# Optimization experiments

Measured on AMD Instinct MI355X. Metric: run time of the kernel, lower is better.

## Reference

```python
import jax, jax.numpy as jnp
import numpy as np

B, D, L = 16, 64, 1280
H = 8            # nhead
WIN = 5          # window_size (divides L exactly)
DFF = 128        # dim_feedforward
EPS = 1e-5


def _layernorm(x, g, b):
    mu = jnp.mean(x, axis=-1, keepdims=True)
    var = jnp.mean(jnp.square(x - mu), axis=-1, keepdims=True)
    return (x - mu) * jax.lax.rsqrt(var + EPS) * g + b


def _mha(x, w_in, b_in, w_out, b_out):
    # x: (Bx, Lx, D). torch nn.MultiheadAttention, batch_first, eval mode.
    Bx, Lx, Dm = x.shape
    hd = Dm // H
    qkv = x @ w_in.T + b_in                      # (Bx, Lx, 3D)
    q, k, v = jnp.split(qkv, 3, axis=-1)
    q = q.reshape(Bx, Lx, H, hd)
    k = k.reshape(Bx, Lx, H, hd)
    v = v.reshape(Bx, Lx, H, hd)
    scale = 1.0 / jnp.sqrt(jnp.asarray(hd, x.dtype))
    scores = jnp.einsum('bqhd,bkhd->bhqk', q, k) * scale
    att = jax.nn.softmax(scores, axis=-1)
    out = jnp.einsum('bhqk,bkhd->bqhd', att, v).reshape(Bx, Lx, Dm)
    return out @ w_out.T + b_out


def setup_inputs() -> dict:
    key = jax.random.key(0)
    ks = jax.random.split(key, 16)
    s = 0.05
    return {
        'x': jax.random.normal(ks[0], (B, D, L), dtype=jnp.float32),
        # local attention params
        'lw_in': jax.random.normal(ks[1], (3 * D, D), dtype=jnp.float32) * s,
        'lb_in': jnp.zeros((3 * D,), jnp.float32),
        'lw_out': jax.random.normal(ks[2], (D, D), dtype=jnp.float32) * s,
        'lb_out': jnp.zeros((D,), jnp.float32),
        # global attention params
        'gw_in': jax.random.normal(ks[3], (3 * D, D), dtype=jnp.float32) * s,
        'gb_in': jnp.zeros((3 * D,), jnp.float32),
        'gw_out': jax.random.normal(ks[4], (D, D), dtype=jnp.float32) * s,
        'gb_out': jnp.zeros((D,), jnp.float32),
        # gating weight (init 0.5 like the module)
        'local_weight': jnp.full((D,), 0.5, jnp.float32),
        # layer norms
        'g1': jnp.ones((D,), jnp.float32), 'b1': jnp.zeros((D,), jnp.float32),
        'g2': jnp.ones((D,), jnp.float32), 'b2': jnp.zeros((D,), jnp.float32),
        'g3': jnp.ones((D,), jnp.float32), 'b3': jnp.zeros((D,), jnp.float32),
        # FFN
        'w1': jax.random.normal(ks[5], (DFF, D), dtype=jnp.float32) * s,
        'bf1': jnp.zeros((DFF,), jnp.float32),
        'w2': jax.random.normal(ks[6], (D, DFF), dtype=jnp.float32) * s,
        'bf2': jnp.zeros((D,), jnp.float32),
    }


def reference(x, lw_in, lb_in, lw_out, lb_out, gw_in, gb_in, gw_out, gb_out,
              local_weight, g1, b1, g2, b2, g3, b3, w1, bf1, w2, bf2):
    xt = jnp.transpose(x, (0, 2, 1))              # (B, L, D)
    residual = xt
    nW = L // WIN
    xw = xt.reshape(B * nW, WIN, D)
    local_out = _mha(xw, lw_in, lb_in, lw_out, lb_out).reshape(B, L, D)
    local_out = _layernorm(local_out + residual, g1, b1)
    # global attention
    global_out = _mha(xt, gw_in, gb_in, gw_out, gb_out)
    global_out = _layernorm(global_out + residual, g2, b2)
    # gated channel fusion
    alpha = jax.nn.sigmoid(local_weight)[None, None, :]
    fused = alpha * local_out + (1.0 - alpha) * global_out
    # FFN (dropout is identity in eval mode)
    ffn_out = jax.nn.relu(fused @ w1.T + bf1) @ w2.T + bf2
    out = _layernorm(ffn_out + fused, g3, b3)
    return jnp.transpose(out, (0, 2, 1))          # (B, D, L)
```

## Files before the change

kernel.cpp:

```cpp
#include <hip/hip_runtime.h>
#include <math.h>

typedef short bf16x8 __attribute__((ext_vector_type(8)));
typedef float f32x4 __attribute__((ext_vector_type(4)));
typedef float f32x16 __attribute__((ext_vector_type(16)));
typedef unsigned short u16;
typedef unsigned int u32;

#define RFL(x) __builtin_amdgcn_readfirstlane(x)

static __device__ __forceinline__ float bf2f(u16 s) {
  union { u32 u; float f; } c; c.u = ((u32)s) << 16; return c.f;
}
static __device__ __forceinline__ u16 f2bf(float f) {
  union { float f; u32 u; } c; c.f = f;
  u32 u = c.u + 0x7fffu + ((c.u >> 16) & 1u);
  return (u16)(u >> 16);
}
static __device__ __forceinline__ u32 pk2(float lo, float hi) {
  u32 r;
  asm("v_cvt_pk_bf16_f32 %0, %1, %2" : "=v"(r) : "v"(lo), "v"(hi));
  return r;
}
static __device__ __forceinline__ f32x4 MF(bf16x8 a, bf16x8 b, f32x4 c) {
  return __builtin_amdgcn_mfma_f32_16x16x32_bf16(a, b, c, 0, 0, 0);
}
static __device__ __forceinline__ f32x16 MF32(bf16x8 a, bf16x8 b, f32x16 c) {
  return __builtin_amdgcn_mfma_f32_32x32x16_bf16(a, b, c, 0, 0, 0);
}


__global__ __launch_bounds__(256) void qkvx(
    const float* __restrict__ x, const float* __restrict__ lw_in,
    const float* __restrict__ gw_in, const float* __restrict__ lb_in,
    const float* __restrict__ gb_in, u16* __restrict__ QKV) {
  __shared__ __align__(16) float xs[32][68];
  __shared__ __align__(16) u16 XTs[32 * 64];
  const int t = threadIdx.x;
  const int b = blockIdx.x / 40, l0 = (blockIdx.x % 40) * 32;
  for (int i = t; i < 2048; i += 256) {
    const int d = i >> 5, tok = i & 31;
    xs[tok][d] = x[(b * 64 + d) * 1280 + l0 + tok];
  }
  __syncthreads();
  {
    const int tok = t >> 3, c8 = (t & 7) * 8;
    union { bf16x8 v; u32 u[4]; } o;
    const float* src = &xs[tok][c8];
    o.u[0] = pk2(src[0], src[1]); o.u[1] = pk2(src[2], src[3]);
    o.u[2] = pk2(src[4], src[5]); o.u[3] = pk2(src[6], src[7]);
    const int byteoff = (tok * 128 + c8 * 2) ^ ((tok & 7) << 4);
    *(bf16x8*)((char*)XTs + byteoff) = o.v;
  }
  __syncthreads();
  const int lane = t & 63, w = RFL(t >> 6);
  const int lr = lane & 15, lg = lane >> 4;
  const int n0 = w * 96;
  bf16x8 a[2][2];
#pragma unroll
  for (int mt = 0; mt < 2; ++mt)
#pragma unroll
    for (int ks = 0; ks < 2; ++ks) {
      const int row = mt * 16 + lr;
      const int abyte = (row * 128 + ks * 64 + lg * 16) ^ ((row & 7) << 4);
      a[mt][ks] = *(const bf16x8*)((char*)XTs + abyte);
    }
  const float* W32 = (n0 < 192) ? lw_in : gw_in;
  const int nb = (n0 < 192) ? n0 : n0 - 192;
  bf16x8 bb[6][2];
#pragma unroll
  for (int nt = 0; nt < 6; ++nt)
#pragma unroll
    for (int ks = 0; ks < 2; ++ks) {
      const float* src = W32 + (nb + nt * 16 + lr) * 64 + ks * 32 + lg * 8;
      const float4 f0 = *(const float4*)src;
      const float4 f1 = *(const float4*)(src + 4);
      union { bf16x8 v; u32 u[4]; } o;
      o.u[0] = pk2(f0.x, f0.y); o.u[1] = pk2(f0.z, f0.w);
      o.u[2] = pk2(f1.x, f1.y); o.u[3] = pk2(f1.z, f1.w);
      bb[nt][ks] = o.v;
    }
  f32x4 acc[2][6];
#pragma unroll
  for (int mt = 0; mt < 2; ++mt)
#pragma unroll
    for (int nt = 0; nt < 6; ++nt) {
      f32x4 z = {0.f, 0.f, 0.f, 0.f};
      acc[mt][nt] = z;
#pragma unroll
      for (int ks = 0; ks < 2; ++ks)
        acc[mt][nt] = MF(a[mt][ks], bb[nt][ks], acc[mt][nt]);
    }
#pragma unroll
  for (int nt = 0; nt < 6; ++nt) {
    const int col = n0 + nt * 16 + lr;
    const float bias = (col < 192) ? lb_in[col] : gb_in[col - 192];
    const float scale = (col < 64) ? 0.35355339059327373f
                      : ((col >= 192 && col < 256) ? 0.51010407600615432f : 1.f);
#pragma unroll
    for (int mt = 0; mt < 2; ++mt)
#pragma unroll
      for (int r = 0; r < 4; ++r) {
        const int row = b * 1280 + l0 + mt * 16 + 4 * lg + r;
        QKV[row * 384 + col] = f2bf((acc[mt][nt][r] + bias) * scale);
      }
  }
}

__global__ __launch_bounds__(512) void attn(
    const u16* __restrict__ QKV, u16* __restrict__ AOl, u16* __restrict__ AOg,
    const float* __restrict__ lw_out, const float* __restrict__ gw_out,
    const float* __restrict__ w1, const float* __restrict__ w2,
    u16* __restrict__ Wlout, u16* __restrict__ Wgout,
    u16* __restrict__ W1b, u16* __restrict__ W2b) {
  __shared__ __align__(16) u16 Klds[1280 * 8];
  __shared__ __align__(16) u16 VT[9 * 1320];
  const int t = threadIdx.x;
  if (blockIdx.x < 5) {
    const int b = blockIdx.y >> 3, h = blockIdx.y & 7;
    for (int l = t; l < 1280; l += 512) {
      const int src = (b * 1280 + l) * 384 + h * 8;
      bf16x8 kv = *(const bf16x8*)(QKV + src + 256);
      bf16x8 vv = *(const bf16x8*)(QKV + src + 320);
      const int k5 = l & 31;
      const int pos = (l & ~31) +
                      ((k5 & 0x13) | ((k5 & 4) << 1) | ((k5 & 8) >> 1));
      *(bf16x8*)(Klds + pos * 8) = kv;
#pragma unroll
      for (int d = 0; d < 8; ++d) VT[d * 1320 + l] = (u16)vv[d];
    }
    for (int l = t; l < 1280; l += 512) VT[8 * 1320 + l] = 0x3F80;
    __syncthreads();
    const int lane = t & 63, w = RFL(t >> 6);
    const int c = lane & 31, hi = lane >> 5;
    const int q0 = blockIdx.x * 256 + w * 32;
    const int qrow = b * 1280 + q0 + c;
    const bf16x8 qv = *(const bf16x8*)(QKV + qrow * 384 + 192 + h * 8);
    const bf16x8 qz = {0, 0, 0, 0, 0, 0, 0, 0};
    const bf16x8 qf = (hi == 0) ? qv : qz;
    const u16* kp = Klds + c * 8;
    const int vrow = (c < 8) ? c : 8;
    const u16* vp = VT + vrow * 1320 + hi * 8;
    f32x16 oacc;
#pragma unroll
    for (int i = 0; i < 16; ++i) oacc[i] = 0.f;
    f32x16 z16;
#pragma unroll
    for (int i = 0; i < 16; ++i) z16[i] = 0.f;
#pragma unroll 2
    for (int jt = 0; jt < 40; ++jt) {
      bf16x8 kf = *(const bf16x8*)kp;
      f32x16 s = MF32(kf, qf, z16);
      float p[16];
#pragma unroll
      for (int i = 0; i < 16; ++i) p[i] = __builtin_amdgcn_exp2f(s[i]);
      union { u32 u[4]; bf16x8 v; } pb1, pb2;
      pb1.u[0] = pk2(p[0], p[1]);  pb1.u[1] = pk2(p[2], p[3]);
      pb1.u[2] = pk2(p[4], p[5]);  pb1.u[3] = pk2(p[6], p[7]);
      pb2.u[0] = pk2(p[8], p[9]);  pb2.u[1] = pk2(p[10], p[11]);
      pb2.u[2] = pk2(p[12], p[13]); pb2.u[3] = pk2(p[14], p[15]);
      bf16x8 vf1 = *(const bf16x8*)vp;
      oacc = MF32(vf1, pb1.v, oacc);
      bf16x8 vf2 = *(const bf16x8*)(vp + 16);
      oacc = MF32(vf2, pb2.v, oacc);
      kp += 256; vp += 32;
    }
    const float ssum = __shfl(oacc[4], c);
    const float inv = 1.f / ssum;
    const int base = qrow * 64 + h * 8 + hi * 4;
    *(u32*)(AOg + base) = pk2(oacc[0] * inv, oacc[1] * inv);
    *(u32*)(AOg + base + 2) = pk2(oacc[2] * inv, oacc[3] * inv);
    return;
  }
  const int lid = (blockIdx.x - 5) * 128 + blockIdx.y;
  if (lid < 320) {
    const int g = lid * 512 + t;
    const int qi = g % 5, h = (g / 5) & 7, wi = (g / 40) & 255, b = g / 10240;
    const int row = b * 1280 + wi * 5 + qi;
    float q[8];
    {
      bf16x8 qv = *(const bf16x8*)(QKV + row * 384 + h * 8);
#pragma unroll
      for (int d = 0; d < 8; ++d) q[d] = bf2f((u16)qv[d]);
    }
    float p[5], sum = 0.f;
#pragma unroll
    for (int j = 0; j < 5; ++j) {
      const int krow = b * 1280 + wi * 5 + j;
      bf16x8 kv = *(const bf16x8*)(QKV + krow * 384 + 64 + h * 8);
      float s = 0.f;
#pragma unroll
      for (int d = 0; d < 8; ++d) s = fmaf(q[d], bf2f((u16)kv[d]), s);
      p[j] = __expf(s); sum += p[j];
    }
    const float inv = 1.f / sum;
    float o[8] = {0, 0, 0, 0, 0, 0, 0, 0};
#pragma unroll
    for (int j = 0; j < 5; ++j) {
      const int vrow = b * 1280 + wi * 5 + j;
      bf16x8 vv = *(const bf16x8*)(QKV + vrow * 384 + 128 + h * 8);
#pragma unroll
      for (int d = 0; d < 8; ++d) o[d] = fmaf(p[j], bf2f((u16)vv[d]), o[d]);
    }
    union { bf16x8 v; u32 u[4]; } ov;
    ov.u[0] = pk2(o[0] * inv, o[1] * inv); ov.u[1] = pk2(o[2] * inv, o[3] * inv);
    ov.u[2] = pk2(o[4] * inv, o[5] * inv); ov.u[3] = pk2(o[6] * inv, o[7] * inv);
    *(bf16x8*)(AOl + row * 64 + h * 8) = ov.v;
  } else {
    const int f = (lid - 320) * 512 + t;
    if (f < 4096)       Wlout[f] = f2bf(lw_out[f]);
    else if (f < 8192)  Wgout[f - 4096] = f2bf(gw_out[f - 4096]);
    else if (f < 16384) W1b[f - 8192] = f2bf(w1[f - 8192]);
    else if (f < 24576) W2b[f - 16384] = f2bf(w2[f - 16384]);
  }
}

__global__ __launch_bounds__(64) void tail_kernel(
    const u16* __restrict__ AOl, const u16* __restrict__ AOg,
    const u16* __restrict__ Wlout, const u16* __restrict__ Wgout,
    const u16* __restrict__ W1b, const u16* __restrict__ W2b,
    const float* __restrict__ lb_out, const float* __restrict__ gb_out,
    const float* __restrict__ lwt,
    const float* __restrict__ g1, const float* __restrict__ b1,
    const float* __restrict__ g2, const float* __restrict__ b2,
    const float* __restrict__ g3, const float* __restrict__ b3,
    const float* __restrict__ bf1, const float* __restrict__ bf2,
    const float* __restrict__ x, float* __restrict__ out) {
  __shared__ __align__(16) float xso[64][20];
  __shared__ __align__(16) u16 Ft[16 * 64];
  __shared__ __align__(16) u16 Ht[16 * 128];
  const int t = threadIdx.x;
  const int b = blockIdx.y, l0 = blockIdx.x * 16;
  for (int i = t; i < 1024; i += 64) {
    const int d = i >> 4, tok = i & 15;
    xso[d][tok] = x[(b * 64 + d) * 1280 + l0 + tok];
  }
  __syncthreads();
  const int lr = t & 15, lg = (t & 63) >> 4;
  const int grow = b * 1280 + l0;

  f32x4 accl[4], accg[4];
#pragma unroll
  for (int nt = 0; nt < 4; ++nt) { f32x4 z = {0,0,0,0}; accl[nt] = z; accg[nt] = z; }
#pragma unroll
  for (int ks = 0; ks < 2; ++ks) {
    bf16x8 al = *(const bf16x8*)(AOl + (grow + lr) * 64 + ks * 32 + lg * 8);
    bf16x8 ag = *(const bf16x8*)(AOg + (grow + lr) * 64 + ks * 32 + lg * 8);
#pragma unroll
    for (int nt = 0; nt < 4; ++nt) {
      bf16x8 bl = *(const bf16x8*)(Wlout + (nt * 16 + lr) * 64 + ks * 32 + lg * 8);
      bf16x8 bg = *(const bf16x8*)(Wgout + (nt * 16 + lr) * 64 + ks * 32 + lg * 8);
      accl[nt] = MF(al, bl, accl[nt]);
      accg[nt] = MF(ag, bg, accg[nt]);
    }
  }
#pragma unroll
  for (int nt = 0; nt < 4; ++nt) {
    const int col = nt * 16 + lr;
    const float bl = lb_out[col], bg = gb_out[col];
    f32x4 xr = *(const f32x4*)&xso[col][lg * 4];
#pragma unroll
    for (int r = 0; r < 4; ++r) {
      accl[nt][r] += bl + xr[r];
      accg[nt][r] += bg + xr[r];
    }
  }
  auto LN = [&](f32x4* a, const float* gam, const float* bet) {
    float gv[4], bv[4];
#pragma unroll
    for (int nt = 0; nt < 4; ++nt) { gv[nt] = gam[nt * 16 + lr]; bv[nt] = bet[nt * 16 + lr]; }
#pragma unroll
    for (int r = 0; r < 4; ++r) {
      float s = a[0][r] + a[1][r] + a[2][r] + a[3][r];
      s += __shfl_xor(s, 1); s += __shfl_xor(s, 2);
      s += __shfl_xor(s, 4); s += __shfl_xor(s, 8);
      const float mu = s * 0.015625f;
      float q = 0.f;
#pragma unroll
      for (int nt = 0; nt < 4; ++nt) { const float cv = a[nt][r] - mu; q = fmaf(cv, cv, q); }
      q += __shfl_xor(q, 1); q += __shfl_xor(q, 2);
      q += __shfl_xor(q, 4); q += __shfl_xor(q, 8);
      const float rsq = rsqrtf(q * 0.015625f + 1e-5f);
#pragma unroll
      for (int nt = 0; nt < 4; ++nt)
        a[nt][r] = (a[nt][r] - mu) * rsq * gv[nt] + bv[nt];
    }
  };
  LN(accl, g1, b1);
  LN(accg, g2, b2);
  f32x4 fus[4];
#pragma unroll
  for (int nt = 0; nt < 4; ++nt) {
    const int col = nt * 16 + lr;
    const float al_ = 1.f / (1.f + __expf(-lwt[col]));
#pragma unroll
    for (int r = 0; r < 4; ++r)
      fus[nt][r] = al_ * accl[nt][r] + (1.f - al_) * accg[nt][r];
  }
#pragma unroll
  for (int nt = 0; nt < 4; ++nt)
#pragma unroll
    for (int r = 0; r < 4; ++r) {
      const int ltok = lg * 4 + r;
      const int byteoff = (ltok * 128 + (nt * 16 + lr) * 2) ^ ((ltok & 7) << 4);
      *(u16*)((char*)Ft + byteoff) = f2bf(fus[nt][r]);
    }
  asm volatile("" ::: "memory");
  __syncthreads();
  f32x4 hcc[8];
#pragma unroll
  for (int nt = 0; nt < 8; ++nt) { f32x4 z = {0,0,0,0}; hcc[nt] = z; }
#pragma unroll
  for (int ks = 0; ks < 2; ++ks) {
    const int abyte = (lr * 128 + ks * 64 + lg * 16) ^ ((lr & 7) << 4);
    bf16x8 af = *(const bf16x8*)((char*)Ft + abyte);
#pragma unroll
    for (int nt = 0; nt < 8; ++nt) {
      bf16x8 bw = *(const bf16x8*)(W1b + (nt * 16 + lr) * 64 + ks * 32 + lg * 8);
      hcc[nt] = MF(af, bw, hcc[nt]);
    }
  }
#pragma unroll
  for (int nt = 0; nt < 8; ++nt) {
    const int f = nt * 16 + lr;
    const float bbv = bf1[f];
#pragma unroll
    for (int r = 0; r < 4; ++r) {
      const float v = fmaxf(hcc[nt][r] + bbv, 0.f);
      const int ltok = lg * 4 + r;
      const int byteoff = (ltok * 256 + f * 2) ^ ((ltok & 7) << 4);
      *(u16*)((char*)Ht + byteoff) = f2bf(v);
    }
  }
  asm volatile("" ::: "memory");
  f32x4 occ[4];
#pragma unroll
  for (int nt = 0; nt < 4; ++nt) { f32x4 z = {0,0,0,0}; occ[nt] = z; }
#pragma unroll
  for (int ks = 0; ks < 4; ++ks) {
    const int abyte = (lr * 256 + ks * 64 + lg * 16) ^ ((lr & 7) << 4);
    bf16x8 af = *(const bf16x8*)((char*)Ht + abyte);
#pragma unroll
    for (int nt = 0; nt < 4; ++nt) {
      bf16x8 bw = *(const bf16x8*)(W2b + (nt * 16 + lr) * 128 + ks * 32 + lg * 8);
      occ[nt] = MF(af, bw, occ[nt]);
    }
  }
#pragma unroll
  for (int nt = 0; nt < 4; ++nt) {
    const float bb2 = bf2[nt * 16 + lr];
#pragma unroll
    for (int r = 0; r < 4; ++r) occ[nt][r] += bb2 + fus[nt][r];
  }
  LN(occ, g3, b3);
#pragma unroll
  for (int nt = 0; nt < 4; ++nt)
#pragma unroll
    for (int r = 0; r < 4; ++r)
      xso[nt * 16 + lr][lg * 4 + r] = occ[nt][r];
  __syncthreads();
  for (int i = t; i < 1024; i += 64) {
    const int d = i >> 4, tok = i & 15;
    out[(b * 64 + d) * 1280 + l0 + tok] = xso[d][tok];
  }
}

extern "C" void kernel_launch(void* const* d_in, const int* in_sizes, int n_in,
                              void* d_out, int out_size, void* d_ws,
                              size_t ws_size, hipStream_t stream) {
  const float* x      = (const float*)d_in[0];
  const float* lw_in  = (const float*)d_in[1];
  const float* lb_in  = (const float*)d_in[2];
  const float* lw_out = (const float*)d_in[3];
  const float* lb_out = (const float*)d_in[4];
  const float* gw_in  = (const float*)d_in[5];
  const float* gb_in  = (const float*)d_in[6];
  const float* gw_out = (const float*)d_in[7];
  const float* gb_out = (const float*)d_in[8];
  const float* lwt    = (const float*)d_in[9];
  const float* g1 = (const float*)d_in[10]; const float* b1 = (const float*)d_in[11];
  const float* g2 = (const float*)d_in[12]; const float* b2 = (const float*)d_in[13];
  const float* g3 = (const float*)d_in[14]; const float* b3 = (const float*)d_in[15];
  const float* w1 = (const float*)d_in[16]; const float* bf1 = (const float*)d_in[17];
  const float* w2 = (const float*)d_in[18]; const float* bf2 = (const float*)d_in[19];
  float* out = (float*)d_out;

  u16* QKV   = (u16*)d_ws;
  u16* AOl   = QKV + 7864320;
  u16* AOg   = AOl + 1310720;
  u16* Wlout = AOg + 1310720;
  u16* Wgout = Wlout + 4096;
  u16* W1b   = Wgout + 4096;
  u16* W2b   = W1b + 8192;

  qkvx<<<dim3(640), dim3(256), 0, stream>>>(x, lw_in, gw_in, lb_in, gb_in, QKV);
  attn<<<dim3(8, 128), dim3(512), 0, stream>>>(QKV, AOl, AOg, lw_out, gw_out,
                                               w1, w2, Wlout, Wgout, W1b, W2b);
  tail_kernel<<<dim3(80, 16), dim3(64), 0, stream>>>(
      AOl, AOg, Wlout, Wgout, W1b, W2b, lb_out, gb_out, lwt,
      g1, b1, g2, b2, g3, b3, bf1, bf2, x, out);
}
```

Before: 77.03 us.

## Split global attention over two key halves and merge partial sums in tail

The global attention is split into two key-range halves per (batch, head, query-block), with 256-thread blocks instead of 512. This gives more blocks and smaller LDS use per block. Each half writes unnormalized fp32 partial outputs and row sums to workspace. The tail kernel adds the two halves and normalizes them, which costs extra global traffic for the fp32 partials. The inner loop also alternates between two accumulators to break the MFMA dependency chain, and it skips the max-subtraction across splits just as before.

```diff
diff --git a/kernel.cpp b/kernel.cpp
--- a/kernel.cpp
+++ b/kernel.cpp
@@ -107,19 +107,23 @@
   }
 }
 
-__global__ __launch_bounds__(512) void attn(
-    const u16* __restrict__ QKV, u16* __restrict__ AOl, u16* __restrict__ AOg,
+__global__ __launch_bounds__(256) void attn(
+    const u16* __restrict__ QKV, u16* __restrict__ AOl,
+    float* __restrict__ OSUM, float* __restrict__ OACC8,
     const float* __restrict__ lw_out, const float* __restrict__ gw_out,
     const float* __restrict__ w1, const float* __restrict__ w2,
     u16* __restrict__ Wlout, u16* __restrict__ Wgout,
     u16* __restrict__ W1b, u16* __restrict__ W2b) {
-  __shared__ __align__(16) u16 Klds[1280 * 8];
-  __shared__ __align__(16) u16 VT[9 * 1320];
+  __shared__ __align__(16) u16 Klds[640 * 8];
+  __shared__ __align__(16) u16 VT[9 * 664];
   const int t = threadIdx.x;
-  if (blockIdx.x < 5) {
-    const int b = blockIdx.y >> 3, h = blockIdx.y & 7;
-    for (int l = t; l < 1280; l += 512) {
-      const int src = (b * 1280 + l) * 384 + h * 8;
+  if (blockIdx.x < 20) {
+    const int bh = blockIdx.y;
+    const int b = bh >> 3, h = bh & 7;
+    const int split = blockIdx.x & 1, qblk = blockIdx.x >> 1;
+    const int k0 = split * 640;
+    for (int l = t; l < 640; l += 256) {
+      const int src = (b * 1280 + k0 + l) * 384 + h * 8;
       bf16x8 kv = *(const bf16x8*)(QKV + src + 256);
       bf16x8 vv = *(const bf16x8*)(QKV + src + 320);
       const int k5 = l & 31;
@@ -127,28 +131,23 @@
                       ((k5 & 0x13) | ((k5 & 4) << 1) | ((k5 & 8) >> 1));
       *(bf16x8*)(Klds + pos * 8) = kv;
 #pragma unroll
-      for (int d = 0; d < 8; ++d) VT[d * 1320 + l] = (u16)vv[d];
-    }
-    for (int l = t; l < 1280; l += 512) VT[8 * 1320 + l] = 0x3F80;
+      for (int d = 0; d < 8; ++d) VT[d * 664 + l] = (u16)vv[d];
+    }
+    for (int l = t; l < 664; l += 256) VT[8 * 664 + l] = 0x3F80;
     __syncthreads();
     const int lane = t & 63, w = RFL(t >> 6);
     const int c = lane & 31, hi = lane >> 5;
-    const int q0 = blockIdx.x * 256 + w * 32;
-    const int qrow = b * 1280 + q0 + c;
-    const bf16x8 qv = *(const bf16x8*)(QKV + qrow * 384 + 192 + h * 8);
+    const int q = qblk * 128 + w * 32 + c;
+    const bf16x8 qv = *(const bf16x8*)(QKV + (b * 1280 + q) * 384 + 192 + h * 8);
     const bf16x8 qz = {0, 0, 0, 0, 0, 0, 0, 0};
     const bf16x8 qf = (hi == 0) ? qv : qz;
     const u16* kp = Klds + c * 8;
     const int vrow = (c < 8) ? c : 8;
-    const u16* vp = VT + vrow * 1320 + hi * 8;
-    f32x16 oacc;
-#pragma unroll
-    for (int i = 0; i < 16; ++i) oacc[i] = 0.f;
-    f32x16 z16;
-#pragma unroll
-    for (int i = 0; i < 16; ++i) z16[i] = 0.f;
-#pragma unroll 2
-    for (int jt = 0; jt < 40; ++jt) {
+    const u16* vp = VT + vrow * 664 + hi * 8;
+    f32x16 oaccA, oaccB, z16;
+#pragma unroll
+    for (int i = 0; i < 16; ++i) { oaccA[i] = 0.f; oaccB[i] = 0.f; z16[i] = 0.f; }
+    auto step = [&](f32x16& oacc) {
       bf16x8 kf = *(const bf16x8*)kp;
       f32x16 s = MF32(kf, qf, z16);
       float p[16];
@@ -164,17 +163,24 @@
       bf16x8 vf2 = *(const bf16x8*)(vp + 16);
       oacc = MF32(vf2, pb2.v, oacc);
       kp += 256; vp += 32;
-    }
-    const float ssum = __shfl(oacc[4], c);
-    const float inv = 1.f / ssum;
-    const int base = qrow * 64 + h * 8 + hi * 4;
-    *(u32*)(AOg + base) = pk2(oacc[0] * inv, oacc[1] * inv);
-    *(u32*)(AOg + base + 2) = pk2(oacc[2] * inv, oacc[3] * inv);
+    };
+#pragma unroll 2
+    for (int jt2 = 0; jt2 < 10; ++jt2) {
+      step(oaccA);
+      step(oaccB);
+    }
+    f32x16 oacc;
+#pragma unroll
+    for (int i = 0; i < 16; ++i) oacc[i] = oaccA[i] + oaccB[i];
+    const int qi = bh * 1280 + q;
+    if (hi == 0) OSUM[split * 163840 + qi] = oacc[4];
+    f32x4 od = {oacc[0], oacc[1], oacc[2], oacc[3]};
+    *(f32x4*)(OACC8 + split * 1310720 + qi * 8 + hi * 4) = od;
     return;
   }
-  const int lid = (blockIdx.x - 5) * 128 + blockIdx.y;
-  if (lid < 320) {
-    const int g = lid * 512 + t;
+  const int lid = (blockIdx.x - 20) * 128 + blockIdx.y;
+  if (lid < 640) {
+    const int g = lid * 256 + t;
     const int qi = g % 5, h = (g / 5) & 7, wi = (g / 40) & 255, b = g / 10240;
     const int row = b * 1280 + wi * 5 + qi;
     float q[8];
@@ -206,8 +212,8 @@
     ov.u[0] = pk2(o[0] * inv, o[1] * inv); ov.u[1] = pk2(o[2] * inv, o[3] * inv);
     ov.u[2] = pk2(o[4] * inv, o[5] * inv); ov.u[3] = pk2(o[6] * inv, o[7] * inv);
     *(bf16x8*)(AOl + row * 64 + h * 8) = ov.v;
-  } else {
-    const int f = (lid - 320) * 512 + t;
+  } else if (lid < 736) {
+    const int f = (lid - 640) * 256 + t;
     if (f < 4096)       Wlout[f] = f2bf(lw_out[f]);
     else if (f < 8192)  Wgout[f - 4096] = f2bf(gw_out[f - 4096]);
     else if (f < 16384) W1b[f - 8192] = f2bf(w1[f - 8192]);
@@ -216,7 +222,8 @@
 }
 
 __global__ __launch_bounds__(64) void tail_kernel(
-    const u16* __restrict__ AOl, const u16* __restrict__ AOg,
+    const u16* __restrict__ AOl,
+    const float* __restrict__ OSUM, const float* __restrict__ OACC8,
     const u16* __restrict__ Wlout, const u16* __restrict__ Wgout,
     const u16* __restrict__ W1b, const u16* __restrict__ W2b,
     const float* __restrict__ lb_out, const float* __restrict__ gb_out,
@@ -245,13 +252,24 @@
 #pragma unroll
   for (int ks = 0; ks < 2; ++ks) {
     bf16x8 al = *(const bf16x8*)(AOl + (grow + lr) * 64 + ks * 32 + lg * 8);
-    bf16x8 ag = *(const bf16x8*)(AOg + (grow + lr) * 64 + ks * 32 + lg * 8);
+    const int h = ks * 4 + lg;
+    const int qi = (b * 8 + h) * 1280 + l0 + lr;
+    f32x4 oa0 = *(const f32x4*)(OACC8 + qi * 8);
+    f32x4 oa1 = *(const f32x4*)(OACC8 + qi * 8 + 4);
+    f32x4 ob0 = *(const f32x4*)(OACC8 + 1310720 + qi * 8);
+    f32x4 ob1 = *(const f32x4*)(OACC8 + 1310720 + qi * 8 + 4);
+    const float inv = 1.f / (OSUM[qi] + OSUM[163840 + qi]);
+    union { bf16x8 v; u32 u[4]; } agv;
+    agv.u[0] = pk2((oa0[0] + ob0[0]) * inv, (oa0[1] + ob0[1]) * inv);
+    agv.u[1] = pk2((oa0[2] + ob0[2]) * inv, (oa0[3] + ob0[3]) * inv);
+    agv.u[2] = pk2((oa1[0] + ob1[0]) * inv, (oa1[1] + ob1[1]) * inv);
+    agv.u[3] = pk2((oa1[2] + ob1[2]) * inv, (oa1[3] + ob1[3]) * inv);
 #pragma unroll
     for (int nt = 0; nt < 4; ++nt) {
       bf16x8 bl = *(const bf16x8*)(Wlout + (nt * 16 + lr) * 64 + ks * 32 + lg * 8);
       bf16x8 bg = *(const bf16x8*)(Wgout + (nt * 16 + lr) * 64 + ks * 32 + lg * 8);
       accl[nt] = MF(al, bl, accl[nt]);
-      accg[nt] = MF(ag, bg, accg[nt]);
+      accg[nt] = MF(agv.v, bg, accg[nt]);
     }
   }
 #pragma unroll
@@ -387,16 +405,18 @@
 
   u16* QKV   = (u16*)d_ws;
   u16* AOl   = QKV + 7864320;
-  u16* AOg   = AOl + 1310720;
-  u16* Wlout = AOg + 1310720;
+  u16* Wlout = AOl + 1310720;
   u16* Wgout = Wlout + 4096;
   u16* W1b   = Wgout + 4096;
   u16* W2b   = W1b + 8192;
+  float* OSUM  = (float*)(W2b + 8192);
+  float* OACC8 = OSUM + 327680;
 
   qkvx<<<dim3(640), dim3(256), 0, stream>>>(x, lw_in, gw_in, lb_in, gb_in, QKV);
-  attn<<<dim3(8, 128), dim3(512), 0, stream>>>(QKV, AOl, AOg, lw_out, gw_out,
-                                               w1, w2, Wlout, Wgout, W1b, W2b);
+  attn<<<dim3(26, 128), dim3(256), 0, stream>>>(QKV, AOl, OSUM, OACC8,
+                                                lw_out, gw_out, w1, w2,
+                                                Wlout, Wgout, W1b, W2b);
   tail_kernel<<<dim3(80, 16), dim3(64), 0, stream>>>(
-      AOl, AOg, Wlout, Wgout, W1b, W2b, lb_out, gb_out, lwt,
+      AOl, OSUM, OACC8, Wlout, Wgout, W1b, W2b, lb_out, gb_out, lwt,
       g1, b1, g2, b2, g3, b3, bf1, bf2, x, out);
 }
```

New measurement: 75.81 us. About the same (-1.6%).
